# Kernel tuning notes

Hardware: AMD Instinct MI355X
Metric: run time of the kernel (lower is better)

The kernel has to match this reference:

```python
import jax, jax.numpy as jnp
import numpy as np

B, T, C, H, D = 2, 2048, 1024, 16, 64

def setup_inputs() -> dict:
    key = jax.random.key(0)
    ks = jax.random.split(key, 5)
    s = 1.0 / np.sqrt(C)
    return {
        "hidden_states": jax.random.normal(ks[0], (B, T, C), jnp.float32),
        "Wq": jax.random.normal(ks[1], (H, C, D), jnp.float32) * s,
        "Wk": jax.random.normal(ks[2], (H, C, D), jnp.float32) * s,
        "Wv": jax.random.normal(ks[3], (H, C, D), jnp.float32) * s,
        "Wo": jax.random.normal(ks[4], (C, C), jnp.float32) * s,
    }

def reference(hidden_states, Wq, Wk, Wv, Wo):
    x = hidden_states  # (B, T, C)
    q = jnp.einsum("btc,hcd->bhtd", x, Wq)
    k = jnp.einsum("btc,hcd->bhtd", x, Wk)
    v = jnp.einsum("btc,hcd->bhtd", x, Wv)
    scale = 1.0 / jnp.sqrt(jnp.asarray(D, x.dtype))
    scores = jnp.einsum("bhtd,bhsd->bhts", q, k) * scale  # (B,H,T,T)
    Tlen = x.shape[1]
    causal = jnp.tril(jnp.ones((Tlen, Tlen), bool))
    scores = jnp.where(causal, scores, jnp.asarray(-jnp.inf, x.dtype))
    probs = jax.nn.softmax(scores, axis=-1)
    heads = jnp.einsum("bhts,bhsd->bhtd", probs, v)  # (B,H,T,D)
    concat = heads.transpose(0, 2, 1, 3).reshape(x.shape[0], Tlen, H * D)  # (B,T,C)
    return jnp.einsum("btc,oc->bto", concat, Wo)  # output projection (dropout=0)
```

## Files before the change

### kernel.cpp

```cpp
#include <hip/hip_runtime.h>
#include <math.h>

#define B_ 2
#define T_ 2048
#define C_ 1024
#define H_ 16
#define D_ 64

typedef short short8 __attribute__((ext_vector_type(8)));
typedef float f32x4 __attribute__((ext_vector_type(4)));
typedef float f32x16 __attribute__((ext_vector_type(16)));

#define LOG2E 1.44269504088896f

__device__ __forceinline__ unsigned short f2bf(float f) {
    unsigned int u = __float_as_uint(f);
    u += 0x7FFFu + ((u >> 16) & 1u);
    return (unsigned short)(u >> 16);
}

#define NCAST 2560

__global__ __launch_bounds__(256) void prep_all(
    const float* __restrict__ x,  const float* __restrict__ Wq,
    const float* __restrict__ Wk, const float* __restrict__ Wv,
    const float* __restrict__ Wo,
    unsigned short* __restrict__ xb,   unsigned short* __restrict__ Wall,
    unsigned short* __restrict__ wob,  int nX, int nW)
{
    const int bid = blockIdx.x;
    const int tid = threadIdx.x;
    if (bid < NCAST) {
        int i = (bid * 256 + tid) * 8;
        const float* s;
        unsigned short* d;
        if (i < nX) { s = x + i; d = xb + i; }
        else {
            int j = i - nX;
            if (j >= nW) return;
            s = Wo + j; d = wob + j;
        }
        float4 a = *(const float4*)s;
        float4 b = *(const float4*)(s + 4);
        ushort4 o0, o1;
        o0.x = f2bf(a.x); o0.y = f2bf(a.y); o0.z = f2bf(a.z); o0.w = f2bf(a.w);
        o1.x = f2bf(b.x); o1.y = f2bf(b.y); o1.z = f2bf(b.z); o1.w = f2bf(b.w);
        *(ushort4*)d = o0;
        *(ushort4*)(d + 4) = o1;
        return;
    }
    __shared__ float t[64][65];
    const int tb = bid - NCAST;
    const int c0 = (tb & 15) * 64;
    const int h  = (tb >> 4) & 15;
    const int z  = tb >> 8;
    const float* W = (z == 0) ? Wq : (z == 1) ? Wk : Wv;
    unsigned short* Wt = Wall + (size_t)z * H_ * D_ * C_;
    const int r = tid >> 4, c4 = (tid & 15) * 4;
    #pragma unroll
    for (int p = 0; p < 4; p++) {
        int cl = r + p * 16;
        float4 v = *(const float4*)&W[((size_t)h * C_ + c0 + cl) * D_ + c4];
        t[cl][c4 + 0] = v.x; t[cl][c4 + 1] = v.y;
        t[cl][c4 + 2] = v.z; t[cl][c4 + 3] = v.w;
    }
    __syncthreads();
    #pragma unroll
    for (int p = 0; p < 4; p++) {
        int d = r + p * 16;
        ushort4 o;
        o.x = f2bf(t[c4 + 0][d]); o.y = f2bf(t[c4 + 1][d]);
        o.z = f2bf(t[c4 + 2][d]); o.w = f2bf(t[c4 + 3][d]);
        *(ushort4*)&Wt[((size_t)h * D_ + d) * C_ + c0 + c4] = o;
    }
}

__global__ __launch_bounds__(256) void qkv_big(
    const unsigned short* __restrict__ X,
    const unsigned short* __restrict__ Wall,
    unsigned short* __restrict__ Qo,
    unsigned short* __restrict__ Ko,
    unsigned short* __restrict__ Vt)
{
    __shared__ unsigned short As[128][72];
    __shared__ unsigned short Bs[128][72];

    const int m0 = blockIdx.x * 128;
    const int n0 = blockIdx.y * 128;
    const int z  = n0 >> 10;
    const int tid = threadIdx.x;
    const int w = tid >> 6, lane = tid & 63, quad = lane >> 4, l16 = lane & 15;
    const int wm = w & 1, wn = w >> 1;
    const int lrow = tid >> 3, lcol = (tid & 7) * 8;

    f32x4 acc[4][4] = {};

    short8 ar[4], br[4];
    #pragma unroll
    for (int p = 0; p < 4; p++) {
        int r = lrow + p * 32;
        ar[p] = *(const short8*)&X[(size_t)(m0 + r) * C_ + lcol];
        br[p] = *(const short8*)&Wall[(size_t)(n0 + r) * C_ + lcol];
    }

    for (int k0 = 0; k0 < C_; k0 += 64) {
        __syncthreads();
        #pragma unroll
        for (int p = 0; p < 4; p++) {
            int r = lrow + p * 32;
            *(short8*)&As[r][lcol] = ar[p];
            *(short8*)&Bs[r][lcol] = br[p];
        }
        __syncthreads();
        if (k0 + 64 < C_) {
            #pragma unroll
            for (int p = 0; p < 4; p++) {
                int r = lrow + p * 32;
                ar[p] = *(const short8*)&X[(size_t)(m0 + r) * C_ + k0 + 64 + lcol];
                br[p] = *(const short8*)&Wall[(size_t)(n0 + r) * C_ + k0 + 64 + lcol];
            }
        }
        #pragma unroll
        for (int ks = 0; ks < 2; ks++) {
            short8 af[4], bf[4];
            #pragma unroll
            for (int i = 0; i < 4; i++)
                af[i] = *(const short8*)&As[wm * 64 + i * 16 + l16][ks * 32 + quad * 8];
            #pragma unroll
            for (int j = 0; j < 4; j++)
                bf[j] = *(const short8*)&Bs[wn * 64 + j * 16 + l16][ks * 32 + quad * 8];
            #pragma unroll
            for (int i = 0; i < 4; i++)
                #pragma unroll
                for (int j = 0; j < 4; j++)
                    acc[i][j] = __builtin_amdgcn_mfma_f32_16x16x32_bf16(af[i], bf[j], acc[i][j], 0, 0, 0);
        }
    }

    if (z == 2) {
        #pragma unroll
        for (int j = 0; j < 4; j++) {
            const int n = n0 + wn * 64 + j * 16 + l16;
            const int h = (n >> 6) & 15, d = n & 63;
            #pragma unroll
            for (int i = 0; i < 4; i++) {
                const int m = m0 + wm * 64 + i * 16 + quad * 4;
                const int b = m >> 11, t = m & (T_ - 1);
                ushort4 pk;
                pk.x = f2bf(acc[i][j][0]);
                pk.y = f2bf(acc[i][j][1]);
                pk.z = f2bf(acc[i][j][2]);
                pk.w = f2bf(acc[i][j][3]);
                *(ushort4*)&Vt[(((size_t)b * H_ + h) * D_ + d) * T_ + t] = pk;
            }
        }
    } else {
        const float scale = (z == 0) ? 0.125f * LOG2E : 1.0f;
        unsigned short* O = (z == 0) ? Qo : Ko;
        #pragma unroll
        for (int j = 0; j < 4; j++) {
            const int n = n0 + wn * 64 + j * 16 + l16;
            const int h = (n >> 6) & 15, d = n & 63;
            #pragma unroll
            for (int i = 0; i < 4; i++)
                #pragma unroll
                for (int r = 0; r < 4; r++) {
                    const int m = m0 + wm * 64 + i * 16 + quad * 4 + r;
                    const int b = m >> 11, t = m & (T_ - 1);
                    O[(((size_t)b * H_ + h) * T_ + t) * D_ + d] = f2bf(acc[i][j][r] * scale);
                }
        }
    }
}

__global__ __launch_bounds__(512, 4) void flash_mfma(
    const unsigned short* __restrict__ Q,
    const unsigned short* __restrict__ K,
    const unsigned short* __restrict__ Vt,
    unsigned short* __restrict__ CC)
{
    __shared__ unsigned short kst[64][72];
    __shared__ unsigned short vts[64][72];
    __shared__ float fob[2][64][68];
    __shared__ float flb_p[2][64];
    __shared__ float flb_t[2][64];

    const int dd   = blockIdx.x;
    const int xs   = dd & 7;
    const int loc  = dd >> 3;
    const int half = loc >> 5, li = loc & 31;
    const int hsub = li & 3, pr = li >> 2;
    const int p    = half ? (15 - pr) : pr;
    const int head = xs * 4 + hsub;
    const int h = head & 15, b = head >> 4;

    const int tid = threadIdx.x;
    const int w = tid >> 6, lane = tid & 63;
    const int l31 = lane & 31, hi = lane >> 5;
    const int wg = w & 3;
    const int g  = w >> 2;
    const int sw = (wg & 1) * 32;
    const int qw = (wg >> 1) * 32;
    const int lrow = tid >> 3, lcol = (tid & 7) * 8;
    const size_t hb  = ((size_t)b * H_ + h) * T_;
    const size_t hbD = ((size_t)b * H_ + h) * D_;

    const int qb  = g ? (31 - p) : p;
    const int q0  = qb * 64;
    const int myn = qb + 1;
    const int nkb = 32 - p;

    short8 qf[4];
    #pragma unroll
    for (int k4 = 0; k4 < 4; k4++)
        qf[k4] = *(const short8*)&Q[(hb + q0 + qw + l31) * D_ + k4 * 16 + hi * 8];

    float l_lane = 0.0f;
    f32x16 o0 = {}, o1 = {};

    short8 kreg, vreg;
    kreg = *(const short8*)&K[(hb + lrow) * D_ + lcol];
    vreg = *(const short8*)&Vt[(hbD + lrow) * T_ + lcol];

    for (int kb = 0; kb < nkb; kb++) {
        __syncthreads();
        *(short8*)&kst[lrow][lcol] = kreg;
        *(short8*)&vts[lrow][lcol] = vreg;
        __syncthreads();
        if (kb + 1 < nkb) {
            const int k0n = (kb + 1) * 64;
            kreg = *(const short8*)&K[(hb + k0n + lrow) * D_ + lcol];
            vreg = *(const short8*)&Vt[(hbD + lrow) * T_ + k0n + lcol];
        }

        if (kb < myn) {
            f32x16 S = {};
            __builtin_amdgcn_s_setprio(1);
            #pragma unroll
            for (int k4 = 0; k4 < 4; k4++) {
                short8 kf = *(const short8*)&kst[sw + l31][k4 * 16 + hi * 8];
                S = __builtin_amdgcn_mfma_f32_32x32x16_bf16(kf, qf[k4], S, 0, 0, 0);
            }
            __builtin_amdgcn_s_setprio(0);

            if (kb == qb) {
                #pragma unroll
                for (int reg = 0; reg < 16; reg++) {
                    const int srel = (reg & 3) + 4 * hi + 8 * (reg >> 2);
                    if (sw + srel > qw + l31) S[reg] = -INFINITY;
                }
            }

            unsigned Wd[8];
            #pragma unroll
            for (int blk = 0; blk < 4; blk++) {
                float e0 = exp2f(S[4 * blk + 0]);
                float e1 = exp2f(S[4 * blk + 1]);
                float e2 = exp2f(S[4 * blk + 2]);
                float e3 = exp2f(S[4 * blk + 3]);
                l_lane += (e0 + e1) + (e2 + e3);
                Wd[2 * blk + 0] = __builtin_amdgcn_perm(
                    __float_as_uint(e1) + 0x8000u, __float_as_uint(e0) + 0x8000u, 0x07060302u);
                Wd[2 * blk + 1] = __builtin_amdgcn_perm(
                    __float_as_uint(e3) + 0x8000u, __float_as_uint(e2) + 0x8000u, 0x07060302u);
            }

            unsigned a0 = Wd[0], b0 = Wd[2];
            asm("v_permlane32_swap_b32 %0, %1" : "+v"(a0), "+v"(b0));
            unsigned a1 = Wd[1], b1 = Wd[3];
            asm("v_permlane32_swap_b32 %0, %1" : "+v"(a1), "+v"(b1));
            unsigned c0 = Wd[4], d0 = Wd[6];
            asm("v_permlane32_swap_b32 %0, %1" : "+v"(c0), "+v"(d0));
            unsigned c1 = Wd[5], d1 = Wd[7];
            asm("v_permlane32_swap_b32 %0, %1" : "+v"(c1), "+v"(d1));
            union { unsigned u[4]; short8 v; } pw0, pw1;
            pw0.u[0] = a0; pw0.u[1] = a1; pw0.u[2] = b0; pw0.u[3] = b1;
            pw1.u[0] = c0; pw1.u[1] = c1; pw1.u[2] = d0; pw1.u[3] = d1;

            __builtin_amdgcn_s_setprio(1);
            {
                short8 vf;
                vf = *(const short8*)&vts[l31][sw + hi * 8];
                o0 = __builtin_amdgcn_mfma_f32_32x32x16_bf16(pw0.v, vf, o0, 0, 0, 0);
                vf = *(const short8*)&vts[l31][sw + 16 + hi * 8];
                o0 = __builtin_amdgcn_mfma_f32_32x32x16_bf16(pw1.v, vf, o0, 0, 0, 0);
                vf = *(const short8*)&vts[32 + l31][sw + hi * 8];
                o1 = __builtin_amdgcn_mfma_f32_32x32x16_bf16(pw0.v, vf, o1, 0, 0, 0);
                vf = *(const short8*)&vts[32 + l31][sw + 16 + hi * 8];
                o1 = __builtin_amdgcn_mfma_f32_32x32x16_bf16(pw1.v, vf, o1, 0, 0, 0);
            }
            __builtin_amdgcn_s_setprio(0);
        }
    }

    l_lane += __shfl_xor(l_lane, 32);

    if (wg & 1) {
        if (lane < 32) flb_p[g][qw + lane] = l_lane;
        #pragma unroll
        for (int reg = 0; reg < 16; reg++) {
            const int qr = (reg & 3) + 4 * hi + 8 * (reg >> 2);
            fob[g][qw + qr][l31]      = o0[reg];
            fob[g][qw + qr][32 + l31] = o1[reg];
        }
    }
    __syncthreads();
    if (!(wg & 1)) {
        const float lt = l_lane + flb_p[g][qw + l31];
        if (lane < 32) flb_t[g][qw + lane] = lt;
        #pragma unroll
        for (int reg = 0; reg < 16; reg++) {
            const int qr = (reg & 3) + 4 * hi + 8 * (reg >> 2);
            const float invl = 1.0f / flb_t[g][qw + qr];
            const float v0 = o0[reg] + fob[g][qw + qr][l31];
            const float v1 = o1[reg] + fob[g][qw + qr][32 + l31];
            const int t = q0 + qw + qr;
            CC[((size_t)b * T_ + t) * C_ + h * D_ + l31]      = f2bf(v0 * invl);
            CC[((size_t)b * T_ + t) * C_ + h * D_ + 32 + l31] = f2bf(v1 * invl);
        }
    }
}

__global__ __launch_bounds__(256) void out_big(
    const unsigned short* __restrict__ X,
    const unsigned short* __restrict__ Wob,
    float* __restrict__ out)
{
    __shared__ unsigned short As[128][72];
    __shared__ unsigned short Bs[128][72];

    const int m0 = blockIdx.x * 128;
    const int n0 = blockIdx.y * 128;
    const int tid = threadIdx.x;
    const int w = tid >> 6, lane = tid & 63, quad = lane >> 4, l16 = lane & 15;
    const int wm = w & 1, wn = w >> 1;
    const int lrow = tid >> 3, lcol = (tid & 7) * 8;

    f32x4 acc[4][4] = {};

    short8 ar[4], br[4];
    #pragma unroll
    for (int p = 0; p < 4; p++) {
        int r = lrow + p * 32;
        ar[p] = *(const short8*)&X[(size_t)(m0 + r) * C_ + lcol];
        br[p] = *(const short8*)&Wob[(size_t)(n0 + r) * C_ + lcol];
    }

    for (int k0 = 0; k0 < C_; k0 += 64) {
        __syncthreads();
        #pragma unroll
        for (int p = 0; p < 4; p++) {
            int r = lrow + p * 32;
            *(short8*)&As[r][lcol] = ar[p];
            *(short8*)&Bs[r][lcol] = br[p];
        }
        __syncthreads();
        if (k0 + 64 < C_) {
            #pragma unroll
            for (int p = 0; p < 4; p++) {
                int r = lrow + p * 32;
                ar[p] = *(const short8*)&X[(size_t)(m0 + r) * C_ + k0 + 64 + lcol];
                br[p] = *(const short8*)&Wob[(size_t)(n0 + r) * C_ + k0 + 64 + lcol];
            }
        }
        #pragma unroll
        for (int ks = 0; ks < 2; ks++) {
            short8 af[4], bf[4];
            #pragma unroll
            for (int i = 0; i < 4; i++)
                af[i] = *(const short8*)&As[wm * 64 + i * 16 + l16][ks * 32 + quad * 8];
            #pragma unroll
            for (int j = 0; j < 4; j++)
                bf[j] = *(const short8*)&Bs[wn * 64 + j * 16 + l16][ks * 32 + quad * 8];
            #pragma unroll
            for (int i = 0; i < 4; i++)
                #pragma unroll
                for (int j = 0; j < 4; j++)
                    acc[i][j] = __builtin_amdgcn_mfma_f32_16x16x32_bf16(af[i], bf[j], acc[i][j], 0, 0, 0);
        }
    }

    #pragma unroll
    for (int i = 0; i < 4; i++)
        #pragma unroll
        for (int j = 0; j < 4; j++)
            #pragma unroll
            for (int r = 0; r < 4; r++)
                out[(size_t)(m0 + wm * 64 + i * 16 + quad * 4 + r) * C_ + n0 + wn * 64 + j * 16 + l16] = acc[i][j][r];
}

extern "C" void kernel_launch(void* const* d_in, const int* in_sizes, int n_in,
                              void* d_out, int out_size, void* d_ws, size_t ws_size,
                              hipStream_t stream) {
    const float* x  = (const float*)d_in[0];
    const float* Wq = (const float*)d_in[1];
    const float* Wk = (const float*)d_in[2];
    const float* Wv = (const float*)d_in[3];
    const float* Wo = (const float*)d_in[4];
    float* out = (float*)d_out;

    const size_t nX = (size_t)B_ * T_ * C_;
    const size_t nW = (size_t)H_ * C_ * D_;
    const size_t nQ = (size_t)B_ * H_ * T_ * D_;
    unsigned short* xb   = (unsigned short*)d_ws;
    unsigned short* Wall = xb + nX;
    unsigned short* Wob  = Wall + 3 * nW;
    unsigned short* Qb   = Wob + nW;
    unsigned short* Kb   = Qb + nQ;
    unsigned short* Vtb  = Kb + nQ;
    unsigned short* CCb  = Vtb + nQ;

    prep_all<<<dim3(NCAST + 768), 256, 0, stream>>>(
        x, Wq, Wk, Wv, Wo, xb, Wall, Wob, (int)nX, (int)nW);
    qkv_big<<<dim3(32, 24), 256, 0, stream>>>(xb, Wall, Qb, Kb, Vtb);
    flash_mfma<<<dim3(512), 512, 0, stream>>>(Qb, Kb, Vtb, CCb);
    out_big<<<dim3(32, 8), 256, 0, stream>>>(CCb, Wob, out);
}
```

Measured before the change: 172.4 us.

## Load QKV GEMM tiles directly into LDS with XOR-swizzled layout

Replaces the register-staged global-to-LDS copy in the QKV projection GEMM with direct global_load_lds 16-byte transfers. The padded LDS layout becomes an unpadded layout with an XOR swizzle on 8-element slots to avoid bank conflicts. This saves VGPRs and the ds_write instructions. However, it drops the register-prefetch overlap, so each k-step's global loads now sit directly before the barrier with no double buffering, which can expose load latency.

```diff
diff --git a/kernel.cpp b/kernel.cpp
--- a/kernel.cpp
+++ b/kernel.cpp
@@ -18,6 +18,10 @@
     u += 0x7FFFu + ((u >> 16) & 1u);
     return (unsigned short)(u >> 16);
 }
+
+#define GLD16(gsrc, ldst) __builtin_amdgcn_global_load_lds( \
+    (const __attribute__((address_space(1))) unsigned int*)(gsrc), \
+    (__attribute__((address_space(3))) unsigned int*)(ldst), 16, 0, 0)
 
 #define NCAST 2560
 
@@ -82,8 +86,8 @@
     unsigned short* __restrict__ Ko,
     unsigned short* __restrict__ Vt)
 {
-    __shared__ unsigned short As[128][72];
-    __shared__ unsigned short Bs[128][72];
+    __shared__ unsigned short As[128 * 64];
+    __shared__ unsigned short Bs[128 * 64];
 
     const int m0 = blockIdx.x * 128;
     const int n0 = blockIdx.y * 128;
@@ -91,44 +95,35 @@
     const int tid = threadIdx.x;
     const int w = tid >> 6, lane = tid & 63, quad = lane >> 4, l16 = lane & 15;
     const int wm = w & 1, wn = w >> 1;
-    const int lrow = tid >> 3, lcol = (tid & 7) * 8;
+    const int srow  = lane >> 3;
+    const int sslot = lane & 7;
 
     f32x4 acc[4][4] = {};
 
-    short8 ar[4], br[4];
-    #pragma unroll
-    for (int p = 0; p < 4; p++) {
-        int r = lrow + p * 32;
-        ar[p] = *(const short8*)&X[(size_t)(m0 + r) * C_ + lcol];
-        br[p] = *(const short8*)&Wall[(size_t)(n0 + r) * C_ + lcol];
-    }
-
     for (int k0 = 0; k0 < C_; k0 += 64) {
         __syncthreads();
         #pragma unroll
         for (int p = 0; p < 4; p++) {
-            int r = lrow + p * 32;
-            *(short8*)&As[r][lcol] = ar[p];
-            *(short8*)&Bs[r][lcol] = br[p];
-        }
-        __syncthreads();
-        if (k0 + 64 < C_) {
-            #pragma unroll
-            for (int p = 0; p < 4; p++) {
-                int r = lrow + p * 32;
-                ar[p] = *(const short8*)&X[(size_t)(m0 + r) * C_ + k0 + 64 + lcol];
-                br[p] = *(const short8*)&Wall[(size_t)(n0 + r) * C_ + k0 + 64 + lcol];
-            }
-        }
+            const int c   = w * 4 + p;
+            const int row = c * 8 + srow;
+            const int gs  = (sslot ^ (row & 7)) * 8;
+            GLD16(&X[(size_t)(m0 + row) * C_ + k0 + gs],    &As[c * 512]);
+            GLD16(&Wall[(size_t)(n0 + row) * C_ + k0 + gs], &Bs[c * 512]);
+        }
+        __syncthreads();
         #pragma unroll
         for (int ks = 0; ks < 2; ks++) {
             short8 af[4], bf[4];
             #pragma unroll
-            for (int i = 0; i < 4; i++)
-                af[i] = *(const short8*)&As[wm * 64 + i * 16 + l16][ks * 32 + quad * 8];
-            #pragma unroll
-            for (int j = 0; j < 4; j++)
-                bf[j] = *(const short8*)&Bs[wn * 64 + j * 16 + l16][ks * 32 + quad * 8];
+            for (int i = 0; i < 4; i++) {
+                const int row = wm * 64 + i * 16 + l16;
+                af[i] = *(const short8*)&As[row * 64 + (((ks * 4 + quad) ^ (row & 7)) << 3)];
+            }
+            #pragma unroll
+            for (int j = 0; j < 4; j++) {
+                const int row = wn * 64 + j * 16 + l16;
+                bf[j] = *(const short8*)&Bs[row * 64 + (((ks * 4 + quad) ^ (row & 7)) << 3)];
+            }
             #pragma unroll
             for (int i = 0; i < 4; i++)
                 #pragma unroll
```

Measured after the change: 176.1 us. 1.02x slower.

## Restructure flash attention into 128-row query blocks with two sequential phases

Applied to the files above, without the earlier changes.

Before, each block paired two 64-row query tiles (p and 31-p) handled by separate wave groups sharing K/V loads. Now each block handles a 128-row query tile with all 8 waves and processes two paired tiles (p and 15-p) one after the other, halving the grid to 256 blocks. This raises K/V reuse per shared-memory load and balances the causal work, but it serialises the two phases, adds an extra pass over K/V, and lowers occupancy through fewer blocks and a changed launch bound.

```diff
diff --git a/kernel.cpp b/kernel.cpp
--- a/kernel.cpp
+++ b/kernel.cpp
@@ -173,7 +173,7 @@
     }
 }
 
-__global__ __launch_bounds__(512, 4) void flash_mfma(
+__global__ __launch_bounds__(512, 2) void flash_mfma(
     const unsigned short* __restrict__ Q,
     const unsigned short* __restrict__ K,
     const unsigned short* __restrict__ Vt,
@@ -181,59 +181,57 @@
 {
     __shared__ unsigned short kst[64][72];
     __shared__ unsigned short vts[64][72];
-    __shared__ float fob[2][64][68];
-    __shared__ float flb_p[2][64];
-    __shared__ float flb_t[2][64];
+    __shared__ float fob[128][68];
+    __shared__ float flb_p[128];
+    __shared__ float flb_t[128];
 
     const int dd   = blockIdx.x;
     const int xs   = dd & 7;
     const int loc  = dd >> 3;
-    const int half = loc >> 5, li = loc & 31;
-    const int hsub = li & 3, pr = li >> 2;
-    const int p    = half ? (15 - pr) : pr;
-    const int head = xs * 4 + hsub;
+    const int head = xs * 4 + (loc & 3);
+    const int p    = loc >> 2;
     const int h = head & 15, b = head >> 4;
 
     const int tid = threadIdx.x;
     const int w = tid >> 6, lane = tid & 63;
     const int l31 = lane & 31, hi = lane >> 5;
-    const int wg = w & 3;
-    const int g  = w >> 2;
-    const int sw = (wg & 1) * 32;
-    const int qw = (wg >> 1) * 32;
+    const int sw = (w & 1) * 32;
+    const int qw = (w >> 1) * 32;
     const int lrow = tid >> 3, lcol = (tid & 7) * 8;
     const size_t hb  = ((size_t)b * H_ + h) * T_;
     const size_t hbD = ((size_t)b * H_ + h) * D_;
 
-    const int qb  = g ? (31 - p) : p;
-    const int q0  = qb * 64;
-    const int myn = qb + 1;
-    const int nkb = 32 - p;
-
-    short8 qf[4];
-    #pragma unroll
-    for (int k4 = 0; k4 < 4; k4++)
-        qf[k4] = *(const short8*)&Q[(hb + q0 + qw + l31) * D_ + k4 * 16 + hi * 8];
-
-    float l_lane = 0.0f;
-    f32x16 o0 = {}, o1 = {};
-
-    short8 kreg, vreg;
-    kreg = *(const short8*)&K[(hb + lrow) * D_ + lcol];
-    vreg = *(const short8*)&Vt[(hbD + lrow) * T_ + lcol];
-
-    for (int kb = 0; kb < nkb; kb++) {
-        __syncthreads();
-        *(short8*)&kst[lrow][lcol] = kreg;
-        *(short8*)&vts[lrow][lcol] = vreg;
-        __syncthreads();
-        if (kb + 1 < nkb) {
-            const int k0n = (kb + 1) * 64;
-            kreg = *(const short8*)&K[(hb + k0n + lrow) * D_ + lcol];
-            vreg = *(const short8*)&Vt[(hbD + lrow) * T_ + k0n + lcol];
-        }
-
-        if (kb < myn) {
+    for (int ph = 0; ph < 2; ph++) {
+        const int qb = ph ? (15 - p) : p;
+        const int q0 = qb * 128;
+        const int niter = 2 * qb + 2;
+
+        short8 qf[4];
+        #pragma unroll
+        for (int k4 = 0; k4 < 4; k4++)
+            qf[k4] = *(const short8*)&Q[(hb + q0 + qw + l31) * D_ + k4 * 16 + hi * 8];
+
+        float l_lane = 0.0f;
+        f32x16 o0 = {}, o1 = {};
+
+        short8 kreg, vreg;
+        kreg = *(const short8*)&K[(hb + lrow) * D_ + lcol];
+        vreg = *(const short8*)&Vt[(hbD + lrow) * T_ + lcol];
+
+        for (int kb = 0; kb < niter; kb++) {
+            __syncthreads();
+            *(short8*)&kst[lrow][lcol] = kreg;
+            *(short8*)&vts[lrow][lcol] = vreg;
+            __syncthreads();
+            if (kb + 1 < niter) {
+                const int k0n = (kb + 1) * 64;
+                kreg = *(const short8*)&K[(hb + k0n + lrow) * D_ + lcol];
+                vreg = *(const short8*)&Vt[(hbD + lrow) * T_ + k0n + lcol];
+            }
+
+            const int s0 = kb * 64 + sw;
+            if (s0 > q0 + qw + 31) continue;
+
             f32x16 S = {};
             __builtin_amdgcn_s_setprio(1);
             #pragma unroll
@@ -243,11 +241,12 @@
             }
             __builtin_amdgcn_s_setprio(0);
 
-            if (kb == qb) {
+            if (kb >= 2 * qb) {
+                const int sg = s0 - q0 - qw;
                 #pragma unroll
                 for (int reg = 0; reg < 16; reg++) {
                     const int srel = (reg & 3) + 4 * hi + 8 * (reg >> 2);
-                    if (sw + srel > qw + l31) S[reg] = -INFINITY;
+                    if (sg + srel > l31) S[reg] = -INFINITY;
                 }
             }
 
@@ -291,32 +290,32 @@
             }
             __builtin_amdgcn_s_setprio(0);
         }
-    }
-
-    l_lane += __shfl_xor(l_lane, 32);
-
-    if (wg & 1) {
-        if (lane < 32) flb_p[g][qw + lane] = l_lane;
-        #pragma unroll
-        for (int reg = 0; reg < 16; reg++) {
-            const int qr = (reg & 3) + 4 * hi + 8 * (reg >> 2);
-            fob[g][qw + qr][l31]      = o0[reg];
-            fob[g][qw + qr][32 + l31] = o1[reg];
-        }
-    }
-    __syncthreads();
-    if (!(wg & 1)) {
-        const float lt = l_lane + flb_p[g][qw + l31];
-        if (lane < 32) flb_t[g][qw + lane] = lt;
-        #pragma unroll
-        for (int reg = 0; reg < 16; reg++) {
-            const int qr = (reg & 3) + 4 * hi + 8 * (reg >> 2);
-            const float invl = 1.0f / flb_t[g][qw + qr];
-            const float v0 = o0[reg] + fob[g][qw + qr][l31];
-            const float v1 = o1[reg] + fob[g][qw + qr][32 + l31];
-            const int t = q0 + qw + qr;
-            CC[((size_t)b * T_ + t) * C_ + h * D_ + l31]      = f2bf(v0 * invl);
-            CC[((size_t)b * T_ + t) * C_ + h * D_ + 32 + l31] = f2bf(v1 * invl);
+
+        l_lane += __shfl_xor(l_lane, 32);
+
+        if (w & 1) {
+            if (lane < 32) flb_p[qw + lane] = l_lane;
+            #pragma unroll
+            for (int reg = 0; reg < 16; reg++) {
+                const int qr = (reg & 3) + 4 * hi + 8 * (reg >> 2);
+                fob[qw + qr][l31]      = o0[reg];
+                fob[qw + qr][32 + l31] = o1[reg];
+            }
+        }
+        __syncthreads();
+        if (!(w & 1)) {
+            const float lt = l_lane + flb_p[qw + l31];
+            if (lane < 32) flb_t[qw + lane] = lt;
+            #pragma unroll
+            for (int reg = 0; reg < 16; reg++) {
+                const int qr = (reg & 3) + 4 * hi + 8 * (reg >> 2);
+                const float invl = 1.0f / flb_t[qw + qr];
+                const float v0 = o0[reg] + fob[qw + qr][l31];
+                const float v1 = o1[reg] + fob[qw + qr][32 + l31];
+                const int t = q0 + qw + qr;
+                CC[((size_t)b * T_ + t) * C_ + h * D_ + l31]      = f2bf(v0 * invl);
+                CC[((size_t)b * T_ + t) * C_ + h * D_ + 32 + l31] = f2bf(v1 * invl);
+            }
         }
     }
 }
@@ -413,6 +412,6 @@
     prep_all<<<dim3(NCAST + 768), 256, 0, stream>>>(
         x, Wq, Wk, Wv, Wo, xb, Wall, Wob, (int)nX, (int)nW);
     qkv_big<<<dim3(32, 24), 256, 0, stream>>>(xb, Wall, Qb, Kb, Vtb);
-    flash_mfma<<<dim3(512), 512, 0, stream>>>(Qb, Kb, Vtb, CCb);
+    flash_mfma<<<dim3(256), 512, 0, stream>>>(Qb, Kb, Vtb, CCb);
     out_big<<<dim3(32, 8), 256, 0, stream>>>(CCb, Wob, out);
 }
```

After: 172.4 us. About the same (+0.0%).

## Double-buffer K/V LDS tiles in flash kernel and remap GEMM blocks across XCDs

Applied to the files above, without the earlier changes.

The flash attention kernel now keeps two LDS buffers for K and V and prefetches two blocks ahead. This drops one of the two barriers per iteration and lets the global loads overlap with the MFMA work. The output staging buffer is placed in a union with the K/V tiles so LDS use stays bounded, and the occupancy hint is lowered from 4 to 2 blocks. Both GEMM kernels remap block IDs so that blocks landing on the same XCD cover contiguous tiles, which should improve L2 reuse. The costs are more LDS per block and possibly fewer resident waves.

```diff
diff --git a/kernel.cpp b/kernel.cpp
--- a/kernel.cpp
+++ b/kernel.cpp
@@ -85,8 +85,10 @@
     __shared__ unsigned short As[128][72];
     __shared__ unsigned short Bs[128][72];
 
-    const int m0 = blockIdx.x * 128;
-    const int n0 = blockIdx.y * 128;
+    const int id = blockIdx.y * 32 + blockIdx.x;
+    const int W  = (id & 7) * 96 + (id >> 3);
+    const int m0 = (W & 31) * 128;
+    const int n0 = (W >> 5) * 128;
     const int z  = n0 >> 10;
     const int tid = threadIdx.x;
     const int w = tid >> 6, lane = tid & 63, quad = lane >> 4, l16 = lane & 15;
@@ -173,15 +175,16 @@
     }
 }
 
-__global__ __launch_bounds__(512, 4) void flash_mfma(
+__global__ __launch_bounds__(512, 2) void flash_mfma(
     const unsigned short* __restrict__ Q,
     const unsigned short* __restrict__ K,
     const unsigned short* __restrict__ Vt,
     unsigned short* __restrict__ CC)
 {
-    __shared__ unsigned short kst[64][72];
-    __shared__ unsigned short vts[64][72];
-    __shared__ float fob[2][64][68];
+    __shared__ union {
+        struct { unsigned short k[2][64][72]; unsigned short v[2][64][72]; } t;
+        float fob[2][64][68];
+    } sm;
     __shared__ float flb_p[2][64];
     __shared__ float flb_t[2][64];
 
@@ -221,14 +224,20 @@
     short8 kreg, vreg;
     kreg = *(const short8*)&K[(hb + lrow) * D_ + lcol];
     vreg = *(const short8*)&Vt[(hbD + lrow) * T_ + lcol];
+    *(short8*)&sm.t.k[0][lrow][lcol] = kreg;
+    *(short8*)&sm.t.v[0][lrow][lcol] = vreg;
+    kreg = *(const short8*)&K[(hb + 64 + lrow) * D_ + lcol];
+    vreg = *(const short8*)&Vt[(hbD + lrow) * T_ + 64 + lcol];
+    __syncthreads();
 
     for (int kb = 0; kb < nkb; kb++) {
-        __syncthreads();
-        *(short8*)&kst[lrow][lcol] = kreg;
-        *(short8*)&vts[lrow][lcol] = vreg;
-        __syncthreads();
+        const int cur = kb & 1;
         if (kb + 1 < nkb) {
-            const int k0n = (kb + 1) * 64;
+            *(short8*)&sm.t.k[cur ^ 1][lrow][lcol] = kreg;
+            *(short8*)&sm.t.v[cur ^ 1][lrow][lcol] = vreg;
+        }
+        if (kb + 2 < nkb) {
+            const int k0n = (kb + 2) * 64;
             kreg = *(const short8*)&K[(hb + k0n + lrow) * D_ + lcol];
             vreg = *(const short8*)&Vt[(hbD + lrow) * T_ + k0n + lcol];
         }
@@ -238,7 +247,7 @@
             __builtin_amdgcn_s_setprio(1);
             #pragma unroll
             for (int k4 = 0; k4 < 4; k4++) {
-                short8 kf = *(const short8*)&kst[sw + l31][k4 * 16 + hi * 8];
+                short8 kf = *(const short8*)&sm.t.k[cur][sw + l31][k4 * 16 + hi * 8];
                 S = __builtin_amdgcn_mfma_f32_32x32x16_bf16(kf, qf[k4], S, 0, 0, 0);
             }
             __builtin_amdgcn_s_setprio(0);
@@ -280,17 +289,18 @@
             __builtin_amdgcn_s_setprio(1);
             {
                 short8 vf;
-                vf = *(const short8*)&vts[l31][sw + hi * 8];
+                vf = *(const short8*)&sm.t.v[cur][l31][sw + hi * 8];
                 o0 = __builtin_amdgcn_mfma_f32_32x32x16_bf16(pw0.v, vf, o0, 0, 0, 0);
-                vf = *(const short8*)&vts[l31][sw + 16 + hi * 8];
+                vf = *(const short8*)&sm.t.v[cur][l31][sw + 16 + hi * 8];
                 o0 = __builtin_amdgcn_mfma_f32_32x32x16_bf16(pw1.v, vf, o0, 0, 0, 0);
-                vf = *(const short8*)&vts[32 + l31][sw + hi * 8];
+                vf = *(const short8*)&sm.t.v[cur][32 + l31][sw + hi * 8];
                 o1 = __builtin_amdgcn_mfma_f32_32x32x16_bf16(pw0.v, vf, o1, 0, 0, 0);
-                vf = *(const short8*)&vts[32 + l31][sw + 16 + hi * 8];
+                vf = *(const short8*)&sm.t.v[cur][32 + l31][sw + 16 + hi * 8];
                 o1 = __builtin_amdgcn_mfma_f32_32x32x16_bf16(pw1.v, vf, o1, 0, 0, 0);
             }
             __builtin_amdgcn_s_setprio(0);
         }
+        __syncthreads();
     }
 
     l_lane += __shfl_xor(l_lane, 32);
@@ -300,8 +310,8 @@
         #pragma unroll
         for (int reg = 0; reg < 16; reg++) {
             const int qr = (reg & 3) + 4 * hi + 8 * (reg >> 2);
-            fob[g][qw + qr][l31]      = o0[reg];
-            fob[g][qw + qr][32 + l31] = o1[reg];
+            sm.fob[g][qw + qr][l31]      = o0[reg];
+            sm.fob[g][qw + qr][32 + l31] = o1[reg];
         }
     }
     __syncthreads();
@@ -312,8 +322,8 @@
         for (int reg = 0; reg < 16; reg++) {
             const int qr = (reg & 3) + 4 * hi + 8 * (reg >> 2);
             const float invl = 1.0f / flb_t[g][qw + qr];
-            const float v0 = o0[reg] + fob[g][qw + qr][l31];
-            const float v1 = o1[reg] + fob[g][qw + qr][32 + l31];
+            const float v0 = o0[reg] + sm.fob[g][qw + qr][l31];
+            const float v1 = o1[reg] + sm.fob[g][qw + qr][32 + l31];
             const int t = q0 + qw + qr;
             CC[((size_t)b * T_ + t) * C_ + h * D_ + l31]      = f2bf(v0 * invl);
             CC[((size_t)b * T_ + t) * C_ + h * D_ + 32 + l31] = f2bf(v1 * invl);
@@ -329,8 +339,10 @@
     __shared__ unsigned short As[128][72];
     __shared__ unsigned short Bs[128][72];
 
-    const int m0 = blockIdx.x * 128;
-    const int n0 = blockIdx.y * 128;
+    const int id = blockIdx.y * 32 + blockIdx.x;
+    const int W  = (id & 7) * 32 + (id >> 3);
+    const int m0 = (W & 31) * 128;
+    const int n0 = (W >> 5) * 128;
     const int tid = threadIdx.x;
     const int w = tid >> 6, lane = tid & 63, quad = lane >> 4, l16 = lane & 15;
     const int wm = w & 1, wn = w >> 1;
```

Measured after the change: 193.1 us. 12.0% more time.
